# Optimization experiments

Hardware: AMD Instinct MI355X
Metric: run time of the kernel (lower is better)

The kernel has to match this reference:

```python
import jax, jax.numpy as jnp
import numpy as np

V_DIM, L_DIM, EMBED, HEADS = 1024, 768, 1024, 16
HEAD_DIM = EMBED // HEADS
SCALE = HEADS ** (-0.5)  # faithful to source: num_heads**-0.5
B, NV, NL = 4, 4096, 256


def _xavier(key, shape):
    fan_in, fan_out = shape[0], shape[1]
    lim = (6.0 / (fan_in + fan_out)) ** 0.5
    return jax.random.uniform(key, shape, jnp.float32, -lim, lim)


def setup_inputs() -> dict:
    key = jax.random.key(0)
    ks = jax.random.split(key, 12)
    inp = {
        'v': jax.random.normal(ks[0], (B, NV, V_DIM), jnp.float32),
        'l': jax.random.normal(ks[1], (B, NL, L_DIM), jnp.float32),
        'attention_mask_l': jnp.ones((B, NL), jnp.int32),
        # weights stored as [in, out] so x @ W
        'W_v2q': _xavier(ks[2], (V_DIM, EMBED)), 'b_v2q': jnp.zeros((EMBED,), jnp.float32),
        'W_l2k': _xavier(ks[3], (L_DIM, EMBED)), 'b_l2k': jnp.zeros((EMBED,), jnp.float32),
        'W_v2v': _xavier(ks[4], (V_DIM, EMBED)), 'b_v2v': jnp.zeros((EMBED,), jnp.float32),
        'W_l2v': _xavier(ks[5], (L_DIM, EMBED)), 'b_l2v': jnp.zeros((EMBED,), jnp.float32),
        'W_v2out': _xavier(ks[6], (EMBED, V_DIM)), 'b_v2out': jnp.zeros((V_DIM,), jnp.float32),
        'W_l2out': _xavier(ks[7], (EMBED, L_DIM)), 'b_l2out': jnp.zeros((L_DIM,), jnp.float32),
    }
    return inp


def _heads(x):
    # [B, N, E] -> [B, H, N, D]
    Bx, N, _ = x.shape
    return x.reshape(Bx, N, HEADS, HEAD_DIM).transpose(0, 2, 1, 3)


def reference(v, l, attention_mask_l, W_v2q, b_v2q, W_l2k, b_l2k, W_v2v, b_v2v,
              W_l2v, b_l2v, W_v2out, b_v2out, W_l2out, b_l2out):
    q = _heads(v @ W_v2q + b_v2q)          # [B,H,Nv,D] vision queries
    k = _heads(l @ W_l2k + b_l2k)          # [B,H,Nl,D] language keys
    val_v = _heads(v @ W_v2v + b_v2v)      # [B,H,Nv,D]
    val_l = _heads(l @ W_l2v + b_l2v)      # [B,H,Nl,D]

    # shared score matrix, reused for both softmax directions
    attn = jnp.einsum('bhqd,bhkd->bhqk', q, k) * SCALE  # [B,H,Nv,Nl]

    # vision attends language: mask invalid language tokens
    mask_bias = jnp.where(attention_mask_l[:, None, None, :] == 0, -1e9, 0.0).astype(attn.dtype)
    attn_v = jax.nn.softmax(attn + mask_bias, axis=-1)   # over Nl
    # language attends vision: softmax over vision axis of the same scores
    attn_l = jax.nn.softmax(attn, axis=-2)               # over Nv

    out_v = jnp.einsum('bhqk,bhkd->bhqd', attn_v, val_l)  # [B,H,Nv,D]
    out_l = jnp.einsum('bhqk,bhqd->bhkd', attn_l, val_v)  # [B,H,Nl,D]

    Bx = v.shape[0]
    out_v = out_v.transpose(0, 2, 1, 3).reshape(Bx, -1, EMBED) @ W_v2out + b_v2out
    out_l = out_l.transpose(0, 2, 1, 3).reshape(Bx, -1, EMBED) @ W_l2out + b_l2out
    return out_v, out_l
```

## Files before the change

kernel.cpp:

```cpp
#include <hip/hip_runtime.h>
#include <hip/hip_bf16.h>

#define EMBED 1024
#define HEADS 16
#define HD 64
#define NVTOK 4096
#define NLTOK 256
#define BATCH 4
#define QSCALE 0.25f

typedef __hip_bfloat16 bf16;
typedef __attribute__((ext_vector_type(8))) short bf16x8;
typedef __attribute__((ext_vector_type(4))) float floatx4;

#define MFMA(a, b, c) __builtin_amdgcn_mfma_f32_16x16x32_bf16((a), (b), (c), 0, 0, 0)

static __device__ __forceinline__ short f2bs(float x) {
  bf16 h = __float2bfloat16(x);
  return *reinterpret_cast<short*>(&h);
}
static __device__ __forceinline__ float b2f(bf16 x) { return __bfloat162float(x); }

typedef const __attribute__((address_space(1))) char ga_char;
typedef __attribute__((address_space(3))) char ls_char;
static __device__ __forceinline__ void load_lds16(const void* g, void* lds) {
  __builtin_amdgcn_global_load_lds((ga_char*)g, (ls_char*)(unsigned)(size_t)(lds), 16, 0, 0);
}

__global__ void detect_dtype(const unsigned* __restrict__ v, int* __restrict__ flag) {
  __shared__ int cnt;
  if (threadIdx.x == 0) cnt = 0;
  __syncthreads();
  unsigned u = v[threadIdx.x];
  int mid = (int)((u >> 7) & 0xFF);
  if (mid >= 110 && mid <= 140) atomicAdd(&cnt, 1);
  __syncthreads();
  if (threadIdx.x == 0) {
    flag[0] = (cnt < 192) ? 1 : 0;
    flag[1] = 0;
  }
}

__global__ void convert_to_bf16_v4(const void* __restrict__ src, bf16* __restrict__ dst,
                                   int n4, const int* __restrict__ flag) {
  int i = blockIdx.x * 256 + threadIdx.x;
  if (i >= n4) return;
  short4 o;
  if (flag[0]) {
    float4 f = ((const float4*)src)[i];
    o.x = f2bs(f.x); o.y = f2bs(f.y); o.z = f2bs(f.z); o.w = f2bs(f.w);
  } else {
    o = ((const short4*)src)[i];
  }
  ((short4*)dst)[i] = o;
}

struct WTArgs {
  const void* src[6];
  bf16* dst[6];
  int R[6];
  int C[6];
  float scale[6];
};
__global__ __launch_bounds__(256) void convert_transpose_all(WTArgs a, const int* __restrict__ flag) {
  __shared__ float tile[32][33];
  const int z = blockIdx.y;
  const int R = a.R[z], C = a.C[z];
  const float sc = a.scale[z];
  const int tpc = C >> 5;
  const int nt = (R >> 5) * tpc;
  const int t = blockIdx.x;
  if (t >= nt) return;
  const int r0 = (t / tpc) << 5, c0 = (t % tpc) << 5;
  {
    const int row = threadIdx.x >> 3, cg = (threadIdx.x & 7) << 2;
    if (flag[0]) {
      float4 f = *(const float4*)((const float*)a.src[z] + (size_t)(r0 + row) * C + c0 + cg);
      tile[row][cg] = f.x * sc; tile[row][cg + 1] = f.y * sc;
      tile[row][cg + 2] = f.z * sc; tile[row][cg + 3] = f.w * sc;
    } else {
      short4 f = *(const short4*)((const short*)a.src[z] + (size_t)(r0 + row) * C + c0 + cg);
      tile[row][cg]     = b2f(*(const bf16*)&f.x) * sc;
      tile[row][cg + 1] = b2f(*(const bf16*)&f.y) * sc;
      tile[row][cg + 2] = b2f(*(const bf16*)&f.z) * sc;
      tile[row][cg + 3] = b2f(*(const bf16*)&f.w) * sc;
    }
  }
  __syncthreads();
  {
    const int col = threadIdx.x >> 3, rg = (threadIdx.x & 7) << 2;
    short4 o;
    o.x = f2bs(tile[rg + 0][col]);
    o.y = f2bs(tile[rg + 1][col]);
    o.z = f2bs(tile[rg + 2][col]);
    o.w = f2bs(tile[rg + 3][col]);
    *(short4*)((short*)a.dst[z] + (size_t)(c0 + col) * R + r0 + rg) = o;
  }
}

struct BArgs {
  const void* src[6];
  bf16* dst[6];
  int n[6];
  float scale[6];
};
__global__ void convert_bias_all(BArgs a, const int* __restrict__ flag) {
  int z = blockIdx.y;
  int i = blockIdx.x * 256 + threadIdx.x;
  if (i >= a.n[z]) return;
  float x = flag[0] ? ((const float*)a.src[z])[i] : b2f(((const bf16*)a.src[z])[i]);
  a.dst[z][i] = __float2bfloat16(x * a.scale[z]);
}

__global__ __launch_bounds__(256) void transpose_vl_heads(const bf16* __restrict__ kv,
                                                          bf16* __restrict__ vlT) {
  __shared__ short t[64][72];
  const int bh = blockIdx.y, b = bh >> 4, h = bh & 15;
  const int nl0 = blockIdx.x << 6;
  const int tid = threadIdx.x;
  {
    const int nl = tid >> 2, dg = (tid & 3) << 4;
    const short* s = (const short*)kv + ((size_t)b * NLTOK + nl0 + nl) * 2048 + 1024 + h * HD + dg;
    *(bf16x8*)&t[nl][dg]     = *(const bf16x8*)s;
    *(bf16x8*)&t[nl][dg + 8] = *(const bf16x8*)(s + 8);
  }
  __syncthreads();
  {
    const int d = tid >> 2, ng = (tid & 3) << 4;
    short* o = (short*)vlT + ((size_t)bh * HD + d) * NLTOK + nl0 + ng;
    short tmp[16];
#pragma unroll
    for (int j = 0; j < 16; j++) tmp[j] = t[ng + j][d];
    *(bf16x8*)o       = *(bf16x8*)&tmp[0];
    *(bf16x8*)(o + 8) = *(bf16x8*)&tmp[8];
  }
}

__global__ __launch_bounds__(256) void gemm_nt(
    const bf16* __restrict__ A, const bf16* __restrict__ Bt,
    const bf16* __restrict__ bias, void* __restrict__ Cout, long long coff,
    int M, int N, int K, float alpha, const int* __restrict__ outf) {
  __shared__ short As[8192];
  __shared__ short Bs[8192];
  const int f32o = outf[0];
  const int tid = threadIdx.x;
  const int wave = tid >> 6, lane = tid & 63;
  const int bm = blockIdx.x * 128, bn = blockIdx.y * 128;
  const int wr = (wave & 1) * 64, wc = (wave >> 1) * 64;
  const int rl = lane & 15, kg = (lane >> 4) * 8;

  const int srow = wave * 16 + (lane >> 2);
  const int scol = (lane & 3) * 8;
  const short* Ag = (const short*)A + (size_t)(bm + srow) * K + scol;
  const short* Bg = (const short*)Bt + (size_t)(bn + srow) * K + scol;
  short* As0l = &As[wave * 512];
  short* As1l = &As[2048 + wave * 512];
  short* As0h = &As[4096 + wave * 512];
  short* As1h = &As[6144 + wave * 512];
  short* Bs0l = &Bs[wave * 512];
  short* Bs1l = &Bs[2048 + wave * 512];
  short* Bs0h = &Bs[4096 + wave * 512];
  short* Bs1h = &Bs[6144 + wave * 512];
  const size_t rstep = (size_t)64 * K;

  floatx4 acc[4][4];
#pragma unroll
  for (int i = 0; i < 4; i++)
#pragma unroll
    for (int j = 0; j < 4; j++) acc[i][j] = (floatx4){0.f, 0.f, 0.f, 0.f};

  for (int k0 = 0; k0 < K; k0 += 64) {
    __syncthreads();
    load_lds16(Ag + k0, As0l);
    load_lds16(Ag + rstep + k0, As1l);
    load_lds16(Ag + k0 + 32, As0h);
    load_lds16(Ag + rstep + k0 + 32, As1h);
    load_lds16(Bg + k0, Bs0l);
    load_lds16(Bg + rstep + k0, Bs1l);
    load_lds16(Bg + k0 + 32, Bs0h);
    load_lds16(Bg + rstep + k0 + 32, Bs1h);
    __syncthreads();
#pragma unroll
    for (int half = 0; half < 2; half++) {
      const short* Ah = &As[half * 4096];
      const short* Bh = &Bs[half * 4096];
      bf16x8 af[4], bfr[4];
#pragma unroll
      for (int i = 0; i < 4; i++) af[i]  = *(const bf16x8*)&Ah[(wr + i * 16 + rl) * 32 + kg];
#pragma unroll
      for (int j = 0; j < 4; j++) bfr[j] = *(const bf16x8*)&Bh[(wc + j * 16 + rl) * 32 + kg];
#pragma unroll
      for (int i = 0; i < 4; i++)
#pragma unroll
        for (int j = 0; j < 4; j++) acc[i][j] = MFMA(af[i], bfr[j], acc[i][j]);
    }
  }

  const int rg = (lane >> 4) * 4;
#pragma unroll
  for (int j = 0; j < 4; j++) {
    int col = bn + wc + j * 16 + rl;
    float bv = b2f(bias[col]);
#pragma unroll
    for (int i = 0; i < 4; i++) {
#pragma unroll
      for (int r = 0; r < 4; r++) {
        int row = bm + wr + i * 16 + rg + r;
        float val = (acc[i][j][r] + bv) * alpha;
        long long idx = coff + (long long)row * N + col;
        if (f32o) ((float*)Cout)[idx] = val;
        else      ((bf16*)Cout)[idx]  = __float2bfloat16(val);
      }
    }
  }
}

__global__ __launch_bounds__(256, 4) void attn_fwd_v(
    const bf16* __restrict__ qv,
    const bf16* __restrict__ kv,
    const bf16* __restrict__ vlT,
    const int* __restrict__ mask,
    bf16* __restrict__ ovh,
    float* __restrict__ sfin) {
  __shared__ short kp_lds[256 * 72];
  __shared__ float stf[1024];
  const int tid = threadIdx.x, wave = tid >> 6, lane = tid & 63;
  const int qt = blockIdx.x, bh = blockIdx.y;
  const int b = bh >> 4, h = bh & 15;
  const size_t qrow0 = (size_t)b * NVTOK + qt * 64;
  const size_t krow0 = (size_t)b * NLTOK;
  const int rl = lane & 15, lg = lane >> 4;

#pragma unroll
  for (int it = 0; it < 8; it++) {
    int vv = it * 256 + tid;
    int nl = vv >> 3, c = vv & 7;
    *(bf16x8*)&kp_lds[nl * 72 + c * 8] =
        *(const bf16x8*)((const short*)kv + (krow0 + nl) * 2048 + h * HD + c * 8);
  }
  kp_lds[tid * 72 + 64] = (short)(mask[b * NLTOK + tid] != 0);
  __syncthreads();

  float mb[16];
#pragma unroll
  for (int ct = 0; ct < 16; ct++)
    mb[ct] = kp_lds[(ct * 16 + rl) * 72 + 64] ? 0.0f : -1e9f;

  floatx4 sacc[16];
#pragma unroll
  for (int ct = 0; ct < 16; ct++) sacc[ct] = (floatx4){0.f, 0.f, 0.f, 0.f};
  const short* qrow = (const short*)qv + (qrow0 + wave * 16 + rl) * 2048 + h * HD;
  bf16x8 a0 = *(const bf16x8*)(qrow + lg * 8);
  bf16x8 a1 = *(const bf16x8*)(qrow + 32 + lg * 8);
#pragma unroll
  for (int ct = 0; ct < 16; ct++) {
    bf16x8 b0 = *(const bf16x8*)&kp_lds[(ct * 16 + rl) * 72 + lg * 8];
    bf16x8 b1 = *(const bf16x8*)&kp_lds[(ct * 16 + rl) * 72 + 32 + lg * 8];
    sacc[ct] = MFMA(a0, b0, sacc[ct]);
    sacc[ct] = MFMA(a1, b1, sacc[ct]);
  }

  const short* vbase = (const short*)vlT + ((size_t)bh * 64 + wave * 16) * 256;
  bf16x8 vfr[8];
#pragma unroll
  for (int ks = 0; ks < 8; ks++)
    vfr[ks] = *(const bf16x8*)(vbase + (size_t)rl * 256 + ks * 32 + lg * 8);

#pragma unroll
  for (int ct = 0; ct < 16; ct++) {
    float s = __expf(sacc[ct][0]) + __expf(sacc[ct][1]) +
              __expf(sacc[ct][2]) + __expf(sacc[ct][3]);
    s += __shfl_xor(s, 16);
    s += __shfl_xor(s, 32);
    if (lane < 16) stf[wave * 256 + ct * 16 + lane] = s;
  }

  float rmax[4] = {-1e30f, -1e30f, -1e30f, -1e30f};
#pragma unroll
  for (int ct = 0; ct < 16; ct++)
#pragma unroll
    for (int r = 0; r < 4; r++) {
      sacc[ct][r] += mb[ct];
      rmax[r] = fmaxf(rmax[r], sacc[ct][r]);
    }
#pragma unroll
  for (int r = 0; r < 4; r++) {
    rmax[r] = fmaxf(rmax[r], __shfl_xor(rmax[r], 1));
    rmax[r] = fmaxf(rmax[r], __shfl_xor(rmax[r], 2));
    rmax[r] = fmaxf(rmax[r], __shfl_xor(rmax[r], 4));
    rmax[r] = fmaxf(rmax[r], __shfl_xor(rmax[r], 8));
  }
  float rsum[4] = {0.f, 0.f, 0.f, 0.f};
#pragma unroll
  for (int ct = 0; ct < 16; ct++)
#pragma unroll
    for (int r = 0; r < 4; r++) {
      sacc[ct][r] = __expf(sacc[ct][r] - rmax[r]);
      rsum[r] += sacc[ct][r];
    }
#pragma unroll
  for (int r = 0; r < 4; r++) {
    rsum[r] += __shfl_xor(rsum[r], 1);
    rsum[r] += __shfl_xor(rsum[r], 2);
    rsum[r] += __shfl_xor(rsum[r], 4);
    rsum[r] += __shfl_xor(rsum[r], 8);
    rsum[r] = 1.0f / fmaxf(rsum[r], 1e-20f);
  }
  __syncthreads();

  {
    float s = stf[tid] + stf[256 + tid] + stf[512 + tid] + stf[768 + tid];
    atomicAdd(&sfin[(size_t)bh * 256 + tid], s);
  }

#pragma unroll
  for (int ct = 0; ct < 16; ct++)
#pragma unroll
    for (int r = 0; r < 4; r++)
      kp_lds[(wave * 16 + lg * 4 + r) * 268 + ct * 16 + rl] = f2bs(sacc[ct][r] * rsum[r]);
  __syncthreads();

  floatx4 oacc[4];
#pragma unroll
  for (int mt = 0; mt < 4; mt++) oacc[mt] = (floatx4){0.f, 0.f, 0.f, 0.f};
#pragma unroll
  for (int ks = 0; ks < 8; ks++) {
#pragma unroll
    for (int mt = 0; mt < 4; mt++) {
      bf16x8 af = *(const bf16x8*)&kp_lds[(mt * 16 + rl) * 268 + ks * 32 + lg * 8];
      oacc[mt] = MFMA(af, vfr[ks], oacc[mt]);
    }
  }
  __syncthreads();

#pragma unroll
  for (int mt = 0; mt < 4; mt++)
#pragma unroll
    for (int r = 0; r < 4; r++)
      kp_lds[(mt * 16 + lg * 4 + r) * 72 + wave * 16 + rl] = f2bs(oacc[mt][r]);
  __syncthreads();

#pragma unroll
  for (int pass = 0; pass < 2; pass++) {
    int idx = pass * 256 + tid;
    int row = idx >> 3, c = idx & 7;
    bf16x8 o = *(const bf16x8*)&kp_lds[row * 72 + c * 8];
    *(bf16x8*)((short*)ovh + (qrow0 + row) * EMBED + h * HD + c * 8) = o;
  }
}

__global__ void zero_f32(float* __restrict__ p, int n) {
  int i = blockIdx.x * 256 + threadIdx.x;
  if (i < n) p[i] = 0.f;
}

__global__ __launch_bounds__(256) void attn_fwd_l(
    const bf16* __restrict__ qv,
    const bf16* __restrict__ kv,
    const float* __restrict__ sf,
    float* __restrict__ olacc) {
  __shared__ short k_lds[256 * 72];
  __shared__ short PT[256 * 40];
  __shared__ short vvT[64 * 40];
  __shared__ float sl[256];
  const int tid = threadIdx.x, wave = tid >> 6, lane = tid & 63;
  const int chunk = blockIdx.x, bh = blockIdx.y;
  const int b = bh >> 4, h = bh & 15;
  const size_t krow0 = (size_t)b * NLTOK;
  const size_t qbase = (size_t)b * NVTOK + chunk * 512;
  const int rl = lane & 15, lg = lane >> 4;

#pragma unroll
  for (int it = 0; it < 8; it++) {
    int vvi = it * 256 + tid;
    int nl = vvi >> 3, c = vvi & 7;
    *(bf16x8*)&k_lds[nl * 72 + c * 8] =
        *(const bf16x8*)((const short*)kv + (krow0 + nl) * 2048 + h * HD + c * 8);
  }
  sl[tid] = 1.0f / fmaxf(sf[(size_t)bh * 256 + tid], 1e-20f);
  __syncthreads();

  floatx4 acc[4][4];
#pragma unroll
  for (int rt = 0; rt < 4; rt++)
#pragma unroll
    for (int dt = 0; dt < 4; dt++) acc[rt][dt] = (floatx4){0.f, 0.f, 0.f, 0.f};

  const int qrt = wave & 1, ctb = (wave >> 1) * 8;
  for (int qs = 0; qs < 16; qs++) {
    const short* qrow = (const short*)qv + (qbase + qs * 32 + qrt * 16 + rl) * 2048 + h * HD;
    bf16x8 a0 = *(const bf16x8*)(qrow + lg * 8);
    bf16x8 a1 = *(const bf16x8*)(qrow + 32 + lg * 8);
    floatx4 s8[8];
#pragma unroll
    for (int i = 0; i < 8; i++) {
      int ct = ctb + i;
      bf16x8 b0 = *(const bf16x8*)&k_lds[(ct * 16 + rl) * 72 + lg * 8];
      bf16x8 b1 = *(const bf16x8*)&k_lds[(ct * 16 + rl) * 72 + 32 + lg * 8];
      floatx4 s = (floatx4){0.f, 0.f, 0.f, 0.f};
      s = MFMA(a0, b0, s);
      s = MFMA(a1, b1, s);
      s8[i] = s;
    }
    __syncthreads();
#pragma unroll
    for (int i = 0; i < 8; i++) {
      int col = (ctb + i) * 16 + rl;
      float linv = sl[col];
#pragma unroll
      for (int r = 0; r < 4; r++)
        PT[col * 40 + qrt * 16 + lg * 4 + r] = f2bs(__expf(s8[i][r]) * linv);
    }
    {
      int qq = tid >> 3, c = tid & 7;
      bf16x8 vvv = *(const bf16x8*)((const short*)qv +
                                    (qbase + qs * 32 + qq) * 2048 + 1024 + h * HD + c * 8);
      const short* vp = (const short*)&vvv;
#pragma unroll
      for (int j = 0; j < 8; j++) vvT[(c * 8 + j) * 40 + qq] = vp[j];
    }
    __syncthreads();
#pragma unroll
    for (int rt = 0; rt < 4; rt++) {
      bf16x8 af = *(const bf16x8*)&PT[(wave * 64 + rt * 16 + rl) * 40 + lg * 8];
#pragma unroll
      for (int dt = 0; dt < 4; dt++) {
        bf16x8 bfr = *(const bf16x8*)&vvT[(dt * 16 + rl) * 40 + lg * 8];
        acc[rt][dt] = MFMA(af, bfr, acc[rt][dt]);
      }
    }
  }
#pragma unroll
  for (int rt = 0; rt < 4; rt++)
#pragma unroll
    for (int dt = 0; dt < 4; dt++)
#pragma unroll
      for (int r = 0; r < 4; r++) {
        int nl = wave * 64 + rt * 16 + lg * 4 + r;
        int d = dt * 16 + rl;
        atomicAdd(&olacc[((size_t)b * NLTOK + nl) * EMBED + h * HD + d], acc[rt][dt][r]);
      }
}

__global__ void finalize_out_l(const float* __restrict__ olacc, bf16* __restrict__ olh) {
  int i = blockIdx.x * 256 + threadIdx.x;
  if (i < 1024 * 1024) olh[i] = __float2bfloat16(olacc[i]);
}

extern "C" void kernel_launch(void* const* d_in, const int* in_sizes, int n_in,
                              void* d_out, int out_size, void* d_ws, size_t ws_size,
                              hipStream_t stream) {
  (void)in_sizes; (void)n_in; (void)out_size; (void)ws_size;
  const void* v_raw = d_in[0];
  const void* l_raw = d_in[1];
  const int*  mask  = (const int*)d_in[2];
  const void* W_v2q = d_in[3];  const void* b_v2q = d_in[4];
  const void* W_l2k = d_in[5];  const void* b_l2k = d_in[6];
  const void* W_v2v = d_in[7];  const void* b_v2v = d_in[8];
  const void* W_l2v = d_in[9];  const void* b_l2v = d_in[10];
  const void* W_v2o = d_in[11]; const void* b_v2o = d_in[12];
  const void* W_l2o = d_in[13]; const void* b_l2o = d_in[14];

  char* ws = (char*)d_ws;
  size_t off = 0;
  auto alloc = [&](size_t bytes) -> void* {
    void* p = ws + off;
    off += (bytes + 255) & ~(size_t)255;
    return p;
  };
  int*  flag   = (int*)alloc(256);
  bf16* vb     = (bf16*)alloc((size_t)16777216 * 2);
  bf16* lb     = (bf16*)alloc((size_t)786432 * 2);
  bf16* b_qv   = (bf16*)alloc(4096);
  bf16* b_kvl  = (bf16*)alloc(4096);
  bf16* bov    = (bf16*)alloc(2048);
  bf16* bol    = (bf16*)alloc(1536);
  bf16* Wqv    = (bf16*)alloc((size_t)2048 * 1024 * 2);
  bf16* Wkvl   = (bf16*)alloc((size_t)2048 * 768 * 2);
  bf16* Wt_v2o = (bf16*)alloc((size_t)1024 * 1024 * 2);
  bf16* Wt_l2o = (bf16*)alloc((size_t)768 * 1024 * 2);
  bf16* qvb    = (bf16*)alloc((size_t)16384 * 2048 * 2);
  bf16* kvb    = (bf16*)alloc((size_t)1024 * 2048 * 2);
  bf16* vlT    = (bf16*)alloc((size_t)64 * 64 * 256 * 2);
  float* sfin  = (float*)alloc((size_t)64 * 256 * 4);
  float* olacc = (float*)alloc((size_t)1024 * 1024 * 4);
  bf16* olh    = (bf16*)alloc((size_t)1024 * 1024 * 2);
  bf16* ovh    = vb;

  detect_dtype<<<1, 256, 0, stream>>>((const unsigned*)v_raw, flag);

  convert_to_bf16_v4<<<16384, 256, 0, stream>>>(v_raw, vb, 4194304, flag);
  convert_to_bf16_v4<<<768, 256, 0, stream>>>(l_raw, lb, 196608, flag);

  BArgs ba;
  ba.src[0] = b_v2q; ba.dst[0] = b_qv;         ba.n[0] = 1024; ba.scale[0] = QSCALE;
  ba.src[1] = b_l2k; ba.dst[1] = b_kvl;        ba.n[1] = 1024; ba.scale[1] = 1.0f;
  ba.src[2] = b_v2v; ba.dst[2] = b_qv + 1024;  ba.n[2] = 1024; ba.scale[2] = 1.0f;
  ba.src[3] = b_l2v; ba.dst[3] = b_kvl + 1024; ba.n[3] = 1024; ba.scale[3] = 1.0f;
  ba.src[4] = b_v2o; ba.dst[4] = bov;          ba.n[4] = 1024; ba.scale[4] = 1.0f;
  ba.src[5] = b_l2o; ba.dst[5] = bol;          ba.n[5] = 768;  ba.scale[5] = 1.0f;
  convert_bias_all<<<dim3(4, 6), 256, 0, stream>>>(ba, flag);

  WTArgs wa;
  wa.src[0] = W_v2q; wa.dst[0] = Wqv;                     wa.R[0] = 1024; wa.C[0] = 1024; wa.scale[0] = QSCALE;
  wa.src[1] = W_l2k; wa.dst[1] = Wkvl;                    wa.R[1] = 768;  wa.C[1] = 1024; wa.scale[1] = 1.0f;
  wa.src[2] = W_v2v; wa.dst[2] = Wqv + (size_t)1024*1024; wa.R[2] = 1024; wa.C[2] = 1024; wa.scale[2] = 1.0f;
  wa.src[3] = W_l2v; wa.dst[3] = Wkvl + (size_t)1024*768; wa.R[3] = 768;  wa.C[3] = 1024; wa.scale[3] = 1.0f;
  wa.src[4] = W_v2o; wa.dst[4] = Wt_v2o;                  wa.R[4] = 1024; wa.C[4] = 1024; wa.scale[4] = 1.0f;
  wa.src[5] = W_l2o; wa.dst[5] = Wt_l2o;                  wa.R[5] = 1024; wa.C[5] = 768;  wa.scale[5] = 1.0f;
  convert_transpose_all<<<dim3(1024, 6), 256, 0, stream>>>(wa, flag);

  zero_f32<<<64, 256, 0, stream>>>(sfin, 64 * 256);
  zero_f32<<<4096, 256, 0, stream>>>(olacc, 1024 * 1024);

  const int* bf16out = flag + 1;
  gemm_nt<<<dim3(128, 16), 256, 0, stream>>>(vb, Wqv, b_qv, qvb, 0, 16384, 2048, 1024, 1.0f, bf16out);
  gemm_nt<<<dim3(8, 16), 256, 0, stream>>>(lb, Wkvl, b_kvl, kvb, 0, 1024, 2048, 768, 1.0f, bf16out);
  transpose_vl_heads<<<dim3(4, 64), 256, 0, stream>>>(kvb, vlT);

  attn_fwd_v<<<dim3(64, 64), 256, 0, stream>>>(qvb, kvb, vlT, mask, ovh, sfin);
  attn_fwd_l<<<dim3(8, 64), 256, 0, stream>>>(qvb, kvb, sfin, olacc);
  finalize_out_l<<<4096, 256, 0, stream>>>(olacc, olh);

  gemm_nt<<<dim3(128, 8), 256, 0, stream>>>(ovh, Wt_v2o, bov, d_out, 0, 16384, 1024, 1024, 1.0f, flag);
  gemm_nt<<<dim3(8, 6), 256, 0, stream>>>(olh, Wt_l2o, bol, d_out, 16777216LL, 1024, 768, 1024, 1.0f, flag);
}
```

Before: 522.0 us.

## Stage GEMM epilogue through LDS for coalesced vector stores; relax attention launch bounds

The GEMM epilogue now writes the bias-added, scaled accumulators into a padded shared-memory tile and then writes them out with coalesced 16-byte vector stores. Before, each lane wrote scalar elements scattered across rows. The fp32 path is done in two halves so the tile fits in the enlarged LDS buffer. The attention kernel's launch-bounds occupancy hint drops from 4 to 3 blocks per CU, giving more registers per thread, and the mask-bias loads move later to shorten register live ranges. The cost is extra LDS traffic and barriers in the epilogue, plus possibly lower occupancy in the attention kernel.

```diff
diff --git a/kernel.cpp b/kernel.cpp
--- a/kernel.cpp
+++ b/kernel.cpp
@@ -140,8 +140,9 @@
     const bf16* __restrict__ A, const bf16* __restrict__ Bt,
     const bf16* __restrict__ bias, void* __restrict__ Cout, long long coff,
     int M, int N, int K, float alpha, const int* __restrict__ outf) {
-  __shared__ short As[8192];
-  __shared__ short Bs[8192];
+  __shared__ short lds_all[16896];
+  short* As = lds_all;
+  short* Bs = lds_all + 8192;
   const int f32o = outf[0];
   const int tid = threadIdx.x;
   const int wave = tid >> 6, lane = tid & 63;
@@ -197,25 +198,56 @@
   }
 
   const int rg = (lane >> 4) * 4;
-#pragma unroll
-  for (int j = 0; j < 4; j++) {
-    int col = bn + wc + j * 16 + rl;
-    float bv = b2f(bias[col]);
-#pragma unroll
-    for (int i = 0; i < 4; i++) {
-#pragma unroll
-      for (int r = 0; r < 4; r++) {
-        int row = bm + wr + i * 16 + rg + r;
-        float val = (acc[i][j][r] + bv) * alpha;
-        long long idx = coff + (long long)row * N + col;
-        if (f32o) ((float*)Cout)[idx] = val;
-        else      ((bf16*)Cout)[idx]  = __float2bfloat16(val);
+  __syncthreads();
+
+  if (!f32o) {
+#pragma unroll
+    for (int j = 0; j < 4; j++) {
+      float bv = b2f(bias[bn + wc + j * 16 + rl]);
+#pragma unroll
+      for (int i = 0; i < 4; i++)
+#pragma unroll
+        for (int r = 0; r < 4; r++)
+          lds_all[(wr + i * 16 + rg + r) * 132 + wc + j * 16 + rl] =
+              f2bs((acc[i][j][r] + bv) * alpha);
+    }
+    __syncthreads();
+#pragma unroll
+    for (int it = 0; it < 8; it++) {
+      int idx = it * 256 + tid;
+      int row = idx >> 4, c = idx & 15;
+      bf16x8 o = *(const bf16x8*)&lds_all[row * 132 + c * 8];
+      *(bf16x8*)((short*)Cout + coff + (long long)(bm + row) * N + bn + c * 8) = o;
+    }
+  } else {
+    float* Cf = (float*)lds_all;
+#pragma unroll
+    for (int p = 0; p < 2; p++) {
+      if ((wave & 1) == p) {
+#pragma unroll
+        for (int j = 0; j < 4; j++) {
+          float bv = b2f(bias[bn + wc + j * 16 + rl]);
+#pragma unroll
+          for (int i = 0; i < 4; i++)
+#pragma unroll
+            for (int r = 0; r < 4; r++)
+              Cf[(i * 16 + rg + r) * 132 + wc + j * 16 + rl] = (acc[i][j][r] + bv) * alpha;
+        }
       }
-    }
-  }
-}
-
-__global__ __launch_bounds__(256, 4) void attn_fwd_v(
+      __syncthreads();
+#pragma unroll
+      for (int it = 0; it < 8; it++) {
+        int idx = it * 256 + tid;
+        int row = idx >> 5, c = idx & 31;
+        float4 o = *(const float4*)&Cf[row * 132 + c * 4];
+        *(float4*)((float*)Cout + coff + (long long)(bm + p * 64 + row) * N + bn + c * 4) = o;
+      }
+      if (p == 0) __syncthreads();
+    }
+  }
+}
+
+__global__ __launch_bounds__(256, 3) void attn_fwd_v(
     const bf16* __restrict__ qv,
     const bf16* __restrict__ kv,
     const bf16* __restrict__ vlT,
@@ -241,11 +273,6 @@
   kp_lds[tid * 72 + 64] = (short)(mask[b * NLTOK + tid] != 0);
   __syncthreads();
 
-  float mb[16];
-#pragma unroll
-  for (int ct = 0; ct < 16; ct++)
-    mb[ct] = kp_lds[(ct * 16 + rl) * 72 + 64] ? 0.0f : -1e9f;
-
   floatx4 sacc[16];
 #pragma unroll
   for (int ct = 0; ct < 16; ct++) sacc[ct] = (floatx4){0.f, 0.f, 0.f, 0.f};
@@ -274,6 +301,11 @@
     s += __shfl_xor(s, 32);
     if (lane < 16) stf[wave * 256 + ct * 16 + lane] = s;
   }
+
+  float mb[16];
+#pragma unroll
+  for (int ct = 0; ct < 16; ct++)
+    mb[ct] = kp_lds[(ct * 16 + rl) * 72 + 64] ? 0.0f : -1e9f;
 
   float rmax[4] = {-1e30f, -1e30f, -1e30f, -1e30f};
 #pragma unroll
```

Result: faster. 489.2 us (-6.3%).
